# Kernel tuning notes

Measured on AMD Instinct MI355X. Metric: run time of the kernel, lower is better.

## Reference

```python
import jax, jax.numpy as jnp
import numpy as np

B, T, C, H = 2, 2048, 1024, 16
HD = C // H
HID = C * 4 // 3  # 1365, SwiGLU hidden
EPS = 1e-5


def _ln(x, g, b):
    m = x.mean(-1, keepdims=True)
    v = ((x - m) ** 2).mean(-1, keepdims=True)
    return (x - m) / jnp.sqrt(v + EPS) * g + b


def setup_inputs() -> dict:
    key0 = jax.random.key(0)
    ks = jax.random.split(key0, 16)
    s = 0.02
    inp = {
        'query': jax.random.normal(ks[0], (B, T, C), jnp.float32),
        'key': jax.random.normal(ks[1], (B, T, C), jnp.float32),
        'g_q': jnp.ones((C,), jnp.float32), 'b_q': jnp.zeros((C,), jnp.float32),
        'g_k': jnp.ones((C,), jnp.float32), 'b_k': jnp.zeros((C,), jnp.float32),
        'in_proj_w': jax.random.normal(ks[2], (3 * C, C), jnp.float32) * s,
        'in_proj_b': jnp.zeros((3 * C,), jnp.float32),
        'out_w': jax.random.normal(ks[3], (C, C), jnp.float32) * s,
        'out_b': jnp.zeros((C,), jnp.float32),
        'proj_w': jax.random.normal(ks[4], (C, C), jnp.float32) * s,
        'proj_b': jnp.zeros((C,), jnp.float32),
        'rel_table': jax.random.normal(ks[5], (H, 2 * 2048 - 1), jnp.float32) * s,
        'g_ffn': jnp.ones((C,), jnp.float32), 'b_ffn': jnp.zeros((C,), jnp.float32),
        'w1': jax.random.normal(ks[6], (HID, C), jnp.float32) * s,
        'w2': jax.random.normal(ks[7], (HID, C), jnp.float32) * s,
        'w3': jax.random.normal(ks[8], (C, HID), jnp.float32) * s,
        'g_out': jnp.ones((C,), jnp.float32), 'b_out': jnp.zeros((C,), jnp.float32),
        'max_len': 2048,
    }
    return inp


def reference(query, key, g_q, b_q, g_k, b_k, in_proj_w, in_proj_b, out_w, out_b,
              proj_w, proj_b, rel_table, g_ffn, b_ffn, w1, w2, w3, g_out, b_out, max_len):
    Tq, Tk = query.shape[1], key.shape[1]
    q = _ln(query, g_q, b_q)
    k = _ln(key, g_k, b_k)
    # in-projection (torch MHA packed weights)
    wq, wk, wv = jnp.split(in_proj_w, 3, axis=0)
    bq, bk, bv = jnp.split(in_proj_b, 3, axis=0)
    qp = (q @ wq.T + bq).reshape(B, Tq, H, HD).transpose(0, 2, 1, 3)
    kp = (k @ wk.T + bk).reshape(B, Tk, H, HD).transpose(0, 2, 1, 3)
    vp = (k @ wv.T + bv).reshape(B, Tk, H, HD).transpose(0, 2, 1, 3)
    # relative-position bias, mean over heads -> [Tq,Tk] additive mask
    rel_idx = jnp.clip(jnp.arange(Tq)[:, None] - jnp.arange(Tk)[None, :] + (max_len - 1),
                       0, 2 * max_len - 2)
    mask = rel_table[:, rel_idx].mean(axis=0)  # [Tq,Tk]
    scores = jnp.einsum('bhqd,bhkd->bhqk', qp, kp) / jnp.sqrt(jnp.float32(HD))
    attn = jax.nn.softmax(scores + mask[None, None], axis=-1)
    ctx = jnp.einsum('bhqk,bhkd->bhqd', attn, vp)
    ctx = ctx.transpose(0, 2, 1, 3).reshape(B, Tq, C)
    attn_out = ctx @ out_w.T + out_b
    attn_out = attn_out @ proj_w.T + proj_b
    x = query + attn_out
    # SwiGLU FFN (proj dropout/dropout are identity at eval)
    h = _ln(x, g_ffn, b_ffn)
    ff = (jax.nn.silu(h @ w1.T) * (h @ w2.T)) @ w3.T
    x = x + ff
    return _ln(x, g_out, b_out)
```

## Files before the change

kernel.cpp:

```cpp
#include <hip/hip_runtime.h>
#include <hip/hip_bf16.h>

static constexpr int Bb  = 2;
static constexpr int Tt  = 2048;
static constexpr int Cc  = 1024;
static constexpr int Hh  = 16;
static constexpr int HDi = 64;
static constexpr int HID = 1365;
static constexpr int HIDP = 1408;
static constexpr int Mm  = Bb * Tt;

typedef unsigned short u16;
typedef __attribute__((ext_vector_type(8))) short bf16x8;
typedef __attribute__((ext_vector_type(4))) float f32x4;
typedef __attribute__((ext_vector_type(8))) unsigned short u16x8;
typedef __attribute__((ext_vector_type(4))) unsigned short u16x4;

__device__ inline u16 f2bf(float f) {
    unsigned u = __builtin_bit_cast(unsigned, f);
    u += 0x7fffu + ((u >> 16) & 1u);
    return (u16)(u >> 16);
}

__device__ inline unsigned cvtpk(float lo, float hi) {
    unsigned r;
    asm("v_cvt_pk_bf16_f32 %0, %1, %2" : "=v"(r) : "v"(lo), "v"(hi));
    return r;
}

__device__ inline float vexp2(float x) {
    float r;
    asm("v_exp_f32 %0, %1" : "=v"(r) : "v"(x));
    return r;
}

__device__ inline void gl16(const void* g, void* l) {
    __builtin_amdgcn_global_load_lds(
        (const __attribute__((address_space(1))) unsigned*)g,
        (__attribute__((address_space(3))) unsigned*)l, 16, 0, 0);
}

template<int OUTBF>
__global__ __launch_bounds__(256) void ln_k(const float* __restrict__ x,
                                            const float* __restrict__ g,
                                            const float* __restrict__ b,
                                            void* __restrict__ yv) {
    int row = blockIdx.x;
    int tid = threadIdx.x;
    const float4* xr = (const float4*)(x + (size_t)row * Cc);
    float4 v = xr[tid];
    float s  = v.x + v.y + v.z + v.w;
    float ss = v.x*v.x + v.y*v.y + v.z*v.z + v.w*v.w;
    __shared__ float rs[256], rq[256];
    rs[tid] = s; rq[tid] = ss;
    __syncthreads();
    for (int o = 128; o > 0; o >>= 1) {
        if (tid < o) { rs[tid] += rs[tid+o]; rq[tid] += rq[tid+o]; }
        __syncthreads();
    }
    float mean = rs[0] * (1.f/Cc);
    float var  = rq[0] * (1.f/Cc) - mean*mean;
    float inv  = rsqrtf(var + 1e-5f);
    float4 gv = ((const float4*)g)[tid];
    float4 bv = ((const float4*)b)[tid];
    float o0 = (v.x-mean)*inv*gv.x + bv.x;
    float o1 = (v.y-mean)*inv*gv.y + bv.y;
    float o2 = (v.z-mean)*inv*gv.z + bv.z;
    float o3 = (v.w-mean)*inv*gv.w + bv.w;
    if (OUTBF) {
        u16x4 o4 = { f2bf(o0), f2bf(o1), f2bf(o2), f2bf(o3) };
        ((u16x4*)((u16*)yv + (size_t)row * Cc))[tid] = o4;
    } else {
        float4 o4 = { o0, o1, o2, o3 };
        ((float4*)((float*)yv + (size_t)row * Cc))[tid] = o4;
    }
}

__global__ __launch_bounds__(256) void ln2_k(const float* __restrict__ q,
                                             const float* __restrict__ k,
                                             const float* __restrict__ gq, const float* __restrict__ bq,
                                             const float* __restrict__ gk, const float* __restrict__ bk,
                                             u16* __restrict__ qn, u16* __restrict__ kn) {
    int row = blockIdx.x;
    const float* x; const float* g; const float* bb; u16* y; int r;
    if (row < Mm) { x = q; g = gq; bb = bq; y = qn; r = row; }
    else          { x = k; g = gk; bb = bk; y = kn; r = row - Mm; }
    int tid = threadIdx.x;
    float4 v = ((const float4*)(x + (size_t)r * Cc))[tid];
    float s  = v.x + v.y + v.z + v.w;
    float ss = v.x*v.x + v.y*v.y + v.z*v.z + v.w*v.w;
    __shared__ float rs[256], rq2[256];
    rs[tid] = s; rq2[tid] = ss;
    __syncthreads();
    for (int o = 128; o > 0; o >>= 1) {
        if (tid < o) { rs[tid] += rs[tid+o]; rq2[tid] += rq2[tid+o]; }
        __syncthreads();
    }
    float mean = rs[0] * (1.f/Cc);
    float var  = rq2[0] * (1.f/Cc) - mean*mean;
    float inv  = rsqrtf(var + 1e-5f);
    float4 gv = ((const float4*)g)[tid];
    float4 bv = ((const float4*)bb)[tid];
    u16x4 o4 = { f2bf((v.x-mean)*inv*gv.x + bv.x), f2bf((v.y-mean)*inv*gv.y + bv.y),
                 f2bf((v.z-mean)*inv*gv.z + bv.z), f2bf((v.w-mean)*inv*gv.w + bv.w) };
    ((u16x4*)(y + (size_t)r * Cc))[tid] = o4;
}

__global__ __launch_bounds__(256) void prep_k(const float* __restrict__ in_proj_w, u16* __restrict__ wA,
                                              const float* __restrict__ proj_w,  u16* __restrict__ wPb,
                                              const float* __restrict__ w1, u16* __restrict__ w1b,
                                              const float* __restrict__ w2, u16* __restrict__ w2b,
                                              const float* __restrict__ w3, u16* __restrict__ w3b,
                                              const float* __restrict__ out_w, u16* __restrict__ wOt,
                                              const float* __restrict__ out_b, const float* __restrict__ bp,
                                              float* __restrict__ bc,
                                              const float* __restrict__ rel, float* __restrict__ mr) {
    __shared__ float sh[64*65];
    int bid = blockIdx.x, tid = threadIdx.x;
    if (bid < 3456) {
        int u = bid * 256 + tid;
        const float* src; u16* dst; int valid;
        if (u < 1536*256)                   { src = in_proj_w; dst = wA;  valid = 3*Cc*Cc; }
        else if ((u -= 1536*256) < 512*256) { src = proj_w;    dst = wPb; valid = Cc*Cc; }
        else if ((u -= 512*256) < 704*256)  { src = w1;        dst = w1b; valid = HID*Cc; }
        else     { u -= 704*256;              src = w2;        dst = w2b; valid = HID*Cc; }
        int e0 = u * 8;
        u16x8 o;
        if (e0 + 8 <= valid) {
            float4 a = *(const float4*)(src + e0);
            float4 b = *(const float4*)(src + e0 + 4);
            o[0]=f2bf(a.x); o[1]=f2bf(a.y); o[2]=f2bf(a.z); o[3]=f2bf(a.w);
            o[4]=f2bf(b.x); o[5]=f2bf(b.y); o[6]=f2bf(b.z); o[7]=f2bf(b.w);
        } else {
            #pragma unroll
            for (int j = 0; j < 8; j++) { int e = e0 + j; o[j] = f2bf(e < valid ? src[e] : 0.f); }
        }
        *(u16x8*)(dst + (size_t)e0) = o;
    } else if (bid < 4160) {
        int idx = (bid - 3456) * 256 + tid;
        int e0 = idx * 8;
        int r = e0 / HIDP, c0 = e0 - r * HIDP;
        u16x8 o;
        #pragma unroll
        for (int j = 0; j < 8; j++) {
            int c = c0 + j;
            o[j] = f2bf(c < HID ? w3[(size_t)r * HID + c] : 0.f);
        }
        *(u16x8*)(w3b + (size_t)e0) = o;
    } else if (bid < 4416) {
        int id = bid - 4160;
        int j0 = (id & 15) * 64, c0 = (id >> 4) * 64;
        #pragma unroll
        for (int i = 0; i < 16; i++) {
            int e = tid + i*256;
            int c = e >> 6, j = e & 63;
            sh[c*65 + j] = out_w[(size_t)(c0 + c) * Cc + j0 + j];
        }
        __syncthreads();
        #pragma unroll
        for (int i = 0; i < 16; i++) {
            int e = tid + i*256;
            int j = e >> 6, c = e & 63;
            wOt[(size_t)(j0 + j) * Cc + c0 + c] = f2bf(sh[c*65 + j]);
        }
    } else if (bid < 5440) {
        int i = bid - 4416;
        float4 w = ((const float4*)(proj_w + (size_t)i * Cc))[tid];
        float4 b = ((const float4*)out_b)[tid];
        float s = w.x*b.x + w.y*b.y + w.z*b.z + w.w*b.w;
        sh[tid] = s; __syncthreads();
        for (int o = 128; o > 0; o >>= 1) {
            if (tid < o) sh[tid] += sh[tid+o];
            __syncthreads();
        }
        if (tid == 0) bc[i] = sh[0] + bp[i];
    } else {
        int j = (bid - 5440) * 256 + tid;
        if (j < 2*Tt - 1) {
            float s = 0.f;
            #pragma unroll
            for (int h = 0; h < Hh; h++) s += rel[(size_t)h * (2*Tt - 1) + j];
            mr[j] = s * (1.f/Hh);
        }
    }
}

template<int OUTBF, int HASRES, int HASBIAS>
__global__ __launch_bounds__(256) void mgemm64_k(const u16* __restrict__ A,
                                                 const u16* __restrict__ W,
                                                 const float* __restrict__ bias,
                                                 const float* __restrict__ res,
                                                 void* __restrict__ outv,
                                                 int N, int K) {
    __shared__ u16 As[2][64*32];
    __shared__ u16 Ws[2][128*32];
    int bm = blockIdx.y * 64, bn = blockIdx.x * 128;
    int tid = threadIdx.x, w = tid >> 6, l = tid & 63;
    int lr = l & 15, lh = l >> 4;
    int wm = (w >> 1) * 32, wn = (w & 1) * 64;
    f32x4 acc[2][4] = {};

    auto stage = [&](int buf, int kt) {
        {
            int row = tid >> 2, slot = tid & 3;
            int ko = kt + ((slot ^ (row & 3)) << 3);
            gl16(A + (size_t)(bm + row) * K + ko, (char*)As[buf] + tid * 16);
        }
        #pragma unroll
        for (int c = 0; c < 2; c++) {
            int i = c*256 + tid;
            int row = i >> 2, slot = i & 3;
            int ko = kt + ((slot ^ (row & 3)) << 3);
            gl16(W + (size_t)(bn + row) * K + ko, (char*)Ws[buf] + (c*256 + tid) * 16);
        }
    };
    stage(0, 0);
    for (int kt = 0; kt < K; kt += 32) {
        int buf = (kt >> 5) & 1;
        __syncthreads();
        if (kt + 32 < K) stage(buf ^ 1, kt + 32);
        bf16x8 af[2], wf[4];
        #pragma unroll
        for (int f = 0; f < 2; f++) {
            int r = wm + f*16 + lr;
            af[f] = *(const bf16x8*)((const char*)As[buf] + r*64 + ((lh ^ (r & 3)) << 4));
        }
        #pragma unroll
        for (int f = 0; f < 4; f++) {
            int rn = wn + f*16 + lr;
            wf[f] = *(const bf16x8*)((const char*)Ws[buf] + rn*64 + ((lh ^ (rn & 3)) << 4));
        }
        #pragma unroll
        for (int fm = 0; fm < 2; fm++)
            #pragma unroll
            for (int fn = 0; fn < 4; fn++)
                acc[fm][fn] = __builtin_amdgcn_mfma_f32_16x16x32_bf16(af[fm], wf[fn], acc[fm][fn], 0, 0, 0);
    }

    #pragma unroll
    for (int fm = 0; fm < 2; fm++) {
        #pragma unroll
        for (int r = 0; r < 4; r++) {
            int row = bm + wm + fm*16 + lh*4 + r;
            #pragma unroll
            for (int fn = 0; fn < 4; fn++) {
                int col = bn + wn + fn*16 + lr;
                float v = acc[fm][fn][r];
                if (HASBIAS) v += bias[col];
                if (HASRES)  v += res[(size_t)row * N + col];
                if (OUTBF) ((u16*)outv)[(size_t)row * N + col] = f2bf(v);
                else       ((float*)outv)[(size_t)row * N + col] = v;
            }
        }
    }
}

__global__ __launch_bounds__(256) void mqkv_k(const u16* __restrict__ qn,
                                              const u16* __restrict__ kn,
                                              const u16* __restrict__ wA,
                                              const float* __restrict__ bias3,
                                              u16* __restrict__ out3,
                                              const u16* __restrict__ wPb,
                                              const u16* __restrict__ wOt,
                                              u16* __restrict__ wCb) {
    int z = blockIdx.z;
    const u16* A; const u16* W; const float* bias = bias3; u16* out;
    if (z < 3) { A = z ? kn : qn; W = wA + (size_t)z * Cc * Cc; bias = bias3 + z * Cc; out = out3 + (size_t)z * Mm * Cc; }
    else       { if (blockIdx.y >= 8) return; A = wPb; W = wOt; out = wCb; }

    __shared__ u16 As[2][128*32];
    __shared__ u16 Ws[2][128*32];
    int bm = blockIdx.y * 128, bn = blockIdx.x * 128;
    int tid = threadIdx.x, w = tid >> 6, l = tid & 63;
    int lr = l & 15, lh = l >> 4;
    int wm = (w >> 1) * 64, wn = (w & 1) * 64;
    f32x4 acc[4][4] = {};

    auto stage = [&](int buf, int kt) {
        #pragma unroll
        for (int c = 0; c < 2; c++) {
            int i = w*128 + c*64 + l;
            int row = i >> 2, slot = i & 3;
            int ko = kt + ((slot ^ (row & 3)) << 3);
            gl16(A + (size_t)(bm + row) * Cc + ko, (char*)As[buf] + (w*128 + c*64) * 16);
            gl16(W + (size_t)(bn + row) * Cc + ko, (char*)Ws[buf] + (w*128 + c*64) * 16);
        }
    };
    stage(0, 0);
    for (int kt = 0; kt < Cc; kt += 32) {
        int buf = (kt >> 5) & 1;
        __syncthreads();
        if (kt + 32 < Cc) stage(buf ^ 1, kt + 32);
        bf16x8 af[4], wf[4];
        #pragma unroll
        for (int f = 0; f < 4; f++) {
            int r = wm + f*16 + lr;
            af[f] = *(const bf16x8*)((const char*)As[buf] + r*64 + ((lh ^ (r & 3)) << 4));
            int rn = wn + f*16 + lr;
            wf[f] = *(const bf16x8*)((const char*)Ws[buf] + rn*64 + ((lh ^ (rn & 3)) << 4));
        }
        #pragma unroll
        for (int fm = 0; fm < 4; fm++)
            #pragma unroll
            for (int fn = 0; fn < 4; fn++)
                acc[fm][fn] = __builtin_amdgcn_mfma_f32_16x16x32_bf16(af[fm], wf[fn], acc[fm][fn], 0, 0, 0);
    }

    #pragma unroll
    for (int fm = 0; fm < 4; fm++) {
        #pragma unroll
        for (int r = 0; r < 4; r++) {
            int row = bm + wm + fm*16 + lh*4 + r;
            #pragma unroll
            for (int fn = 0; fn < 4; fn++) {
                int col = bn + wn + fn*16 + lr;
                float v = acc[fm][fn][r];
                if (z < 3) v += bias[col];
                out[(size_t)row * Cc + col] = f2bf(v);
            }
        }
    }
}

__global__ __launch_bounds__(256) void mswiglu64_k(const u16* __restrict__ A,
                                                   const u16* __restrict__ W1,
                                                   const u16* __restrict__ W2,
                                                   u16* __restrict__ out,
                                                   int N, int K) {
    __shared__ u16 As[2][64*32];
    __shared__ u16 W1s[2][128*32];
    __shared__ u16 W2s[2][128*32];
    int bm = blockIdx.y * 64, bn = blockIdx.x * 128;
    int tid = threadIdx.x, w = tid >> 6, l = tid & 63;
    int lr = l & 15, lh = l >> 4;
    int wm = (w >> 1) * 32, wn = (w & 1) * 64;
    f32x4 acc1[2][4] = {};
    f32x4 acc2[2][4] = {};

    auto stage = [&](int buf, int kt) {
        {
            int row = tid >> 2, slot = tid & 3;
            int ko = kt + ((slot ^ (row & 3)) << 3);
            gl16(A + (size_t)(bm + row) * K + ko, (char*)As[buf] + tid * 16);
        }
        #pragma unroll
        for (int c = 0; c < 2; c++) {
            int i = c*256 + tid;
            int row = i >> 2, slot = i & 3;
            int ko = kt + ((slot ^ (row & 3)) << 3);
            gl16(W1 + (size_t)(bn + row) * K + ko, (char*)W1s[buf] + (c*256 + tid) * 16);
            gl16(W2 + (size_t)(bn + row) * K + ko, (char*)W2s[buf] + (c*256 + tid) * 16);
        }
    };
    stage(0, 0);
    for (int kt = 0; kt < K; kt += 32) {
        int buf = (kt >> 5) & 1;
        __syncthreads();
        if (kt + 32 < K) stage(buf ^ 1, kt + 32);
        bf16x8 af[2], w1f[4], w2f[4];
        #pragma unroll
        for (int f = 0; f < 2; f++) {
            int r = wm + f*16 + lr;
            af[f] = *(const bf16x8*)((const char*)As[buf] + r*64 + ((lh ^ (r & 3)) << 4));
        }
        #pragma unroll
        for (int f = 0; f < 4; f++) {
            int rn = wn + f*16 + lr;
            int offn = rn*64 + ((lh ^ (rn & 3)) << 4);
            w1f[f] = *(const bf16x8*)((const char*)W1s[buf] + offn);
            w2f[f] = *(const bf16x8*)((const char*)W2s[buf] + offn);
        }
        #pragma unroll
        for (int fm = 0; fm < 2; fm++)
            #pragma unroll
            for (int fn = 0; fn < 4; fn++) {
                acc1[fm][fn] = __builtin_amdgcn_mfma_f32_16x16x32_bf16(af[fm], w1f[fn], acc1[fm][fn], 0, 0, 0);
                acc2[fm][fn] = __builtin_amdgcn_mfma_f32_16x16x32_bf16(af[fm], w2f[fn], acc2[fm][fn], 0, 0, 0);
            }
    }

    #pragma unroll
    for (int fm = 0; fm < 2; fm++) {
        #pragma unroll
        for (int r = 0; r < 4; r++) {
            int row = bm + wm + fm*16 + lh*4 + r;
            #pragma unroll
            for (int fn = 0; fn < 4; fn++) {
                int col = bn + wn + fn*16 + lr;
                float a = acc1[fm][fn][r];
                float sig = 1.f / (1.f + __expf(-a));
                out[(size_t)row * N + col] = f2bf(a * sig * acc2[fm][fn][r]);
            }
        }
    }
}

__global__ __launch_bounds__(256) void vt_k(const u16* __restrict__ vp,
                                            u16* __restrict__ vt) {
    int blk = blockIdx.x;
    int bh = blk >> 5, kb = blk & 31;
    int b = bh >> 4, h = bh & 15;
    __shared__ u16 t[64][65];
    int tid = threadIdx.x;
    size_t bc = (size_t)b*Tt*Cc + (size_t)h*HDi;
    #pragma unroll
    for (int i = 0; i < 16; i++) {
        int e = tid + i*256;
        int k = e >> 6, d = e & 63;
        t[d][k] = vp[bc + (size_t)(kb*64 + k)*Cc + d];
    }
    __syncthreads();
    #pragma unroll
    for (int i = 0; i < 16; i++) {
        int e = tid + i*256;
        int d = e >> 6, k = e & 63;
        vt[((size_t)bh*64 + d)*Tt + kb*64 + k] = t[d][k];
    }
}

__global__ __launch_bounds__(512) void fattn_k(const u16* __restrict__ qp,
                                               const u16* __restrict__ kp,
                                               const u16* __restrict__ vt,
                                               const float* __restrict__ mr,
                                               u16* __restrict__ ctx) {
    __shared__ alignas(128) u16 Kt[2*4096];
    __shared__ alignas(128) u16 Vts[2*4096];
    __shared__ float mrw[2176];

    constexpr float C1 = 0.18033688011118324f;

    int bid = blockIdx.x;
    int blk = ((bid & 7) << 6) | (bid >> 3);
    int qt = blk & 15, h = (blk >> 4) & 15, b = blk >> 8;
    int q0 = qt * 128;
    int tid = threadIdx.x, w = tid >> 6, l = tid & 63;
    int lr = l & 15, lh = l >> 4;
    size_t bc = (size_t)b * Tt * Cc + (size_t)h * HDi;
    const u16* vtb = vt + (size_t)(b*Hh + h) * HDi * Tt;

    for (int i = tid; i < 2175; i += 512) mrw[i] = mr[q0 + i] * 8.f;

    bf16x8 qa[2];
    {
        const u16* qrow = qp + bc + (size_t)(q0 + w*16 + lr) * Cc;
        qa[0] = *(const bf16x8*)(qrow + lh*8);
        qa[1] = *(const bf16x8*)(qrow + 32 + lh*8);
    }

    f32x4 oacc[4] = {};
    float mrun = -1e30f, lrun = 0.f;

    const char* pKb0 = (const char*)Kt + (lr>>2)*1024 + (lr&3)*128
                       + ((lh ^ (lr & 3)) << 4) + (((lr >> 2) & 1) << 6);
    const char* pKb1 = (const char*)((size_t)pKb0 ^ 64);
    int g6 = ((((lr >> 2) ^ (lr >> 3)) & 1) << 6);
    const char* pV0 = (const char*)Vts + lr*128 + ((lh ^ (lr & 3)) << 4) + g6;
    const char* pV1 = (const char*)((size_t)pV0 ^ 64);
    const char* pm = (const char*)mrw + (w*16 + lr - lh*8 + 2047 - 39) * 4;

    int sl = tid & 7, kr0 = tid >> 3;
    int so = (sl ^ (kr0 & 7) ^ (((kr0 >> 3) & 1) << 2)) << 3;
    const u16* gK = kp + bc + (size_t)kr0 * Cc + so;
    const u16* gV = vtb + (size_t)kr0 * Tt + so;
    int wb = (tid & 448) * 16;
    char* dK0 = (char*)Kt  + wb;
    char* dV0 = (char*)Vts + wb;

    auto stage = [&](int bufo) {
        gl16(gK, dK0 + bufo);
        gl16(gV, dV0 + bufo);
        gK += 64*Cc;
        gV += 64;
    };

    auto tile = [&](int bufo) {
        f32x4 s[4];
        #pragma unroll
        for (int f = 0; f < 4; f++) {
            int ob = 39 - (f & 1)*32 - (f >> 1)*4;
            s[f][0] = *(const float*)(pm + (ob    ) * 4);
            s[f][1] = *(const float*)(pm + (ob - 1) * 4);
            s[f][2] = *(const float*)(pm + (ob - 2) * 4);
            s[f][3] = *(const float*)(pm + (ob - 3) * 4);
        }
        pm -= 256;
        __builtin_amdgcn_s_setprio(1);
        {
            const char* k0 = pKb0 + bufo;
            const char* k1 = pKb1 + bufo;
            bf16x8 kb;
            kb = *(const bf16x8*)(k0 + 0);    s[0] = __builtin_amdgcn_mfma_f32_16x16x32_bf16(kb, qa[0], s[0], 0, 0, 0);
            kb = *(const bf16x8*)(k1 + 0);    s[0] = __builtin_amdgcn_mfma_f32_16x16x32_bf16(kb, qa[1], s[0], 0, 0, 0);
            kb = *(const bf16x8*)(k0 + 4096); s[1] = __builtin_amdgcn_mfma_f32_16x16x32_bf16(kb, qa[0], s[1], 0, 0, 0);
            kb = *(const bf16x8*)(k1 + 4096); s[1] = __builtin_amdgcn_mfma_f32_16x16x32_bf16(kb, qa[1], s[1], 0, 0, 0);
            kb = *(const bf16x8*)(k1 + 512);  s[2] = __builtin_amdgcn_mfma_f32_16x16x32_bf16(kb, qa[0], s[2], 0, 0, 0);
            kb = *(const bf16x8*)(k0 + 512);  s[2] = __builtin_amdgcn_mfma_f32_16x16x32_bf16(kb, qa[1], s[2], 0, 0, 0);
            kb = *(const bf16x8*)(k1 + 4608); s[3] = __builtin_amdgcn_mfma_f32_16x16x32_bf16(kb, qa[0], s[3], 0, 0, 0);
            kb = *(const bf16x8*)(k0 + 4608); s[3] = __builtin_amdgcn_mfma_f32_16x16x32_bf16(kb, qa[1], s[3], 0, 0, 0);
        }
        __builtin_amdgcn_s_setprio(0);

        float tm = -1e30f;
        #pragma unroll
        for (int f = 0; f < 4; f++)
            #pragma unroll
            for (int r = 0; r < 4; r++) tm = fmaxf(tm, s[f][r]);
        tm = fmaxf(tm, __shfl_xor(tm, 16));
        tm = fmaxf(tm, __shfl_xor(tm, 32));

        float corr = 1.f;
        bool nod = __all(tm <= mrun + 64.f);
        if (!nod) {
            float mn = fmaxf(mrun, tm);
            corr = vexp2((mrun - mn) * C1);
            mrun = mn;
        }
        float mnc = mrun * C1;
        float ts = 0.f;
        #pragma unroll
        for (int f = 0; f < 4; f++)
            #pragma unroll
            for (int r = 0; r < 4; r++) {
                float e = vexp2(fmaf(s[f][r], C1, -mnc));
                s[f][r] = e; ts += e;
            }
        ts += __shfl_xor(ts, 16);
        ts += __shfl_xor(ts, 32);
        if (nod) {
            lrun += ts;
        } else {
            lrun = lrun*corr + ts;
            #pragma unroll
            for (int f = 0; f < 4; f++) {
                oacc[f][0] *= corr; oacc[f][1] *= corr;
                oacc[f][2] *= corr; oacc[f][3] *= corr;
            }
        }

        uint4 pb0u = { cvtpk(s[0][0], s[0][1]), cvtpk(s[0][2], s[0][3]),
                       cvtpk(s[2][0], s[2][1]), cvtpk(s[2][2], s[2][3]) };
        uint4 pb1u = { cvtpk(s[1][0], s[1][1]), cvtpk(s[1][2], s[1][3]),
                       cvtpk(s[3][0], s[3][1]), cvtpk(s[3][2], s[3][3]) };
        bf16x8 pb0 = __builtin_bit_cast(bf16x8, pb0u);
        bf16x8 pb1 = __builtin_bit_cast(bf16x8, pb1u);

        __builtin_amdgcn_s_setprio(1);
        #pragma unroll
        for (int f = 0; f < 4; f++) {
            bf16x8 vb0 = *(const bf16x8*)(pV0 + bufo + f*2048);
            oacc[f] = __builtin_amdgcn_mfma_f32_16x16x32_bf16(vb0, pb0, oacc[f], 0, 0, 0);
            bf16x8 vb1 = *(const bf16x8*)(pV1 + bufo + f*2048);
            oacc[f] = __builtin_amdgcn_mfma_f32_16x16x32_bf16(vb1, pb1, oacc[f], 0, 0, 0);
        }
        __builtin_amdgcn_s_setprio(0);
    };

    stage(0);
    #pragma unroll 1
    for (int kt = 0; kt < 32; kt += 2) {
        __syncthreads();
        stage(8192);
        tile(0);
        __syncthreads();
        if (kt < 30) stage(0);
        tile(8192);
    }

    float iv = 1.f / lrun;
    size_t rowoff = bc + (size_t)(q0 + w*16 + lr) * Cc;
    #pragma unroll
    for (int f = 0; f < 4; f++) {
        u16x4 o4 = { f2bf(oacc[f][0]*iv), f2bf(oacc[f][1]*iv),
                     f2bf(oacc[f][2]*iv), f2bf(oacc[f][3]*iv) };
        *(u16x4*)(ctx + rowoff + f*16 + lh*4) = o4;
    }
}

extern "C" void kernel_launch(void* const* d_in, const int* in_sizes, int n_in,
                              void* d_out, int out_size, void* d_ws, size_t ws_size,
                              hipStream_t stream) {
    const float* query     = (const float*)d_in[0];
    const float* key       = (const float*)d_in[1];
    const float* g_q       = (const float*)d_in[2];
    const float* b_q       = (const float*)d_in[3];
    const float* g_k       = (const float*)d_in[4];
    const float* b_k       = (const float*)d_in[5];
    const float* in_proj_w = (const float*)d_in[6];
    const float* in_proj_b = (const float*)d_in[7];
    const float* out_w     = (const float*)d_in[8];
    const float* out_b     = (const float*)d_in[9];
    const float* proj_w    = (const float*)d_in[10];
    const float* proj_b    = (const float*)d_in[11];
    const float* rel_table = (const float*)d_in[12];
    const float* g_ffn     = (const float*)d_in[13];
    const float* b_ffn     = (const float*)d_in[14];
    const float* w1        = (const float*)d_in[15];
    const float* w2        = (const float*)d_in[16];
    const float* w3        = (const float*)d_in[17];
    const float* g_out     = (const float*)d_in[18];
    const float* b_out     = (const float*)d_in[19];

    char* p = (char*)d_ws;
    auto alloc = [&](size_t bytes) { char* r = p; p += bytes; return r; };
    const size_t MCb = (size_t)Mm * Cc * 2;
    u16* wA  = (u16*)alloc((size_t)3*Cc*Cc*2);
    u16* wPb = (u16*)alloc((size_t)Cc*Cc*2);
    u16* wOt = (u16*)alloc((size_t)Cc*Cc*2);
    u16* wCb = (u16*)alloc((size_t)Cc*Cc*2);
    u16* w1b = (u16*)alloc((size_t)HIDP*Cc*2);
    u16* w2b = (u16*)alloc((size_t)HIDP*Cc*2);
    u16* w3b = (u16*)alloc((size_t)Cc*HIDP*2);
    float* bc = (float*)alloc(Cc*4);
    float* mr = (float*)alloc(4096*4);
    u16* qn = (u16*)alloc(MCb);
    u16* kn = (u16*)alloc(MCb);
    u16* qp = (u16*)alloc(MCb);
    u16* kp = (u16*)alloc(MCb);
    u16* vp = (u16*)alloc(MCb);
    u16* vt = (u16*)alloc(MCb);
    float* x  = (float*)alloc((size_t)Mm*Cc*4);
    float* x2 = (float*)alloc((size_t)Mm*Cc*4);
    u16* ctx = qn;
    u16* h   = qp;
    u16* gf  = vp;

    dim3 blk(256);
    prep_k<<<5456, blk, 0, stream>>>(in_proj_w, wA, proj_w, wPb, w1, w1b, w2, w2b,
                                     w3, w3b, out_w, wOt, out_b, proj_b, bc, rel_table, mr);

    ln2_k<<<2*Mm, blk, 0, stream>>>(query, key, g_q, b_q, g_k, b_k, qn, kn);

    dim3 gqkv(Cc/128, Mm/128, 4);
    mqkv_k<<<gqkv, blk, 0, stream>>>(qn, kn, wA, in_proj_b, qp, wPb, wOt, wCb);

    vt_k<<<Bb*Hh*32, blk, 0, stream>>>(vp, vt);
    fattn_k<<<Bb*Hh*16, dim3(512), 0, stream>>>(qp, kp, vt, mr, ctx);

    dim3 g1(Cc/128, Mm/64);
    mgemm64_k<0,1,1><<<g1, blk, 0, stream>>>(ctx, wCb, bc, query, x, Cc, Cc);

    ln_k<1><<<Mm, blk, 0, stream>>>(x, g_ffn, b_ffn, h);
    dim3 g2(HIDP/128, Mm/64);
    mswiglu64_k<<<g2, blk, 0, stream>>>(h, w1b, w2b, gf, HIDP, Cc);
    dim3 g3(Cc/128, Mm/64);
    mgemm64_k<0,1,0><<<g3, blk, 0, stream>>>(gf, w3b, nullptr, x, x2, Cc, HIDP);

    ln_k<0><<<Mm, blk, 0, stream>>>(x2, g_out, b_out, d_out);
}
```

Baseline: 256.9 us.

## Fuse LN into prep kernel, remap QKV grid for XCDs, widen attention KV tile

The query/key layernorm kernel is merged into the weight-prep kernel, which saves one launch. The QKV GEMM now uses a 1D grid of 832 blocks whose block IDs are remapped so neighbouring tiles land on the same XCD, and it drops the dead blocks the old z=3 slice produced. The flash-attention kernel processes 128 keys per iteration instead of 64, doubling the K/V LDS buffers and halving the number of loop iterations and barriers. The larger LDS footprint and register count may lower occupancy.

```diff
diff --git a/kernel.cpp b/kernel.cpp
--- a/kernel.cpp
+++ b/kernel.cpp
@@ -76,47 +76,47 @@
     }
 }
 
-__global__ __launch_bounds__(256) void ln2_k(const float* __restrict__ q,
-                                             const float* __restrict__ k,
-                                             const float* __restrict__ gq, const float* __restrict__ bq,
-                                             const float* __restrict__ gk, const float* __restrict__ bk,
-                                             u16* __restrict__ qn, u16* __restrict__ kn) {
-    int row = blockIdx.x;
-    const float* x; const float* g; const float* bb; u16* y; int r;
-    if (row < Mm) { x = q; g = gq; bb = bq; y = qn; r = row; }
-    else          { x = k; g = gk; bb = bk; y = kn; r = row - Mm; }
-    int tid = threadIdx.x;
-    float4 v = ((const float4*)(x + (size_t)r * Cc))[tid];
-    float s  = v.x + v.y + v.z + v.w;
-    float ss = v.x*v.x + v.y*v.y + v.z*v.z + v.w*v.w;
-    __shared__ float rs[256], rq2[256];
-    rs[tid] = s; rq2[tid] = ss;
-    __syncthreads();
-    for (int o = 128; o > 0; o >>= 1) {
-        if (tid < o) { rs[tid] += rs[tid+o]; rq2[tid] += rq2[tid+o]; }
-        __syncthreads();
-    }
-    float mean = rs[0] * (1.f/Cc);
-    float var  = rq2[0] * (1.f/Cc) - mean*mean;
-    float inv  = rsqrtf(var + 1e-5f);
-    float4 gv = ((const float4*)g)[tid];
-    float4 bv = ((const float4*)bb)[tid];
-    u16x4 o4 = { f2bf((v.x-mean)*inv*gv.x + bv.x), f2bf((v.y-mean)*inv*gv.y + bv.y),
-                 f2bf((v.z-mean)*inv*gv.z + bv.z), f2bf((v.w-mean)*inv*gv.w + bv.w) };
-    ((u16x4*)(y + (size_t)r * Cc))[tid] = o4;
-}
-
-__global__ __launch_bounds__(256) void prep_k(const float* __restrict__ in_proj_w, u16* __restrict__ wA,
-                                              const float* __restrict__ proj_w,  u16* __restrict__ wPb,
-                                              const float* __restrict__ w1, u16* __restrict__ w1b,
-                                              const float* __restrict__ w2, u16* __restrict__ w2b,
-                                              const float* __restrict__ w3, u16* __restrict__ w3b,
-                                              const float* __restrict__ out_w, u16* __restrict__ wOt,
-                                              const float* __restrict__ out_b, const float* __restrict__ bp,
-                                              float* __restrict__ bc,
-                                              const float* __restrict__ rel, float* __restrict__ mr) {
+__global__ __launch_bounds__(256) void prepln_k(const float* __restrict__ query,
+                                                const float* __restrict__ key,
+                                                const float* __restrict__ gq, const float* __restrict__ bq,
+                                                const float* __restrict__ gk, const float* __restrict__ bk,
+                                                u16* __restrict__ qn, u16* __restrict__ kn,
+                                                const float* __restrict__ in_proj_w, u16* __restrict__ wA,
+                                                const float* __restrict__ proj_w,  u16* __restrict__ wPb,
+                                                const float* __restrict__ w1, u16* __restrict__ w1b,
+                                                const float* __restrict__ w2, u16* __restrict__ w2b,
+                                                const float* __restrict__ w3, u16* __restrict__ w3b,
+                                                const float* __restrict__ out_w, u16* __restrict__ wOt,
+                                                const float* __restrict__ out_b, const float* __restrict__ bp,
+                                                float* __restrict__ bc,
+                                                const float* __restrict__ rel, float* __restrict__ mr) {
     __shared__ float sh[64*65];
     int bid = blockIdx.x, tid = threadIdx.x;
+    if (bid < 2*Mm) {
+        const float* x; const float* g; const float* bb; u16* y; int r;
+        if (bid < Mm) { x = query; g = gq; bb = bq; y = qn; r = bid; }
+        else          { x = key;   g = gk; bb = bk; y = kn; r = bid - Mm; }
+        float4 v = ((const float4*)(x + (size_t)r * Cc))[tid];
+        float s  = v.x + v.y + v.z + v.w;
+        float ss = v.x*v.x + v.y*v.y + v.z*v.z + v.w*v.w;
+        float* rs = sh; float* rq2 = sh + 256;
+        rs[tid] = s; rq2[tid] = ss;
+        __syncthreads();
+        for (int o = 128; o > 0; o >>= 1) {
+            if (tid < o) { rs[tid] += rs[tid+o]; rq2[tid] += rq2[tid+o]; }
+            __syncthreads();
+        }
+        float mean = rs[0] * (1.f/Cc);
+        float var  = rq2[0] * (1.f/Cc) - mean*mean;
+        float inv  = rsqrtf(var + 1e-5f);
+        float4 gv = ((const float4*)g)[tid];
+        float4 bv = ((const float4*)bb)[tid];
+        u16x4 o4 = { f2bf((v.x-mean)*inv*gv.x + bv.x), f2bf((v.y-mean)*inv*gv.y + bv.y),
+                     f2bf((v.z-mean)*inv*gv.z + bv.z), f2bf((v.w-mean)*inv*gv.w + bv.w) };
+        ((u16x4*)(y + (size_t)r * Cc))[tid] = o4;
+        return;
+    }
+    bid -= 2*Mm;
     if (bid < 3456) {
         int u = bid * 256 + tid;
         const float* src; u16* dst; int valid;
@@ -263,14 +263,24 @@
                                               const u16* __restrict__ wPb,
                                               const u16* __restrict__ wOt,
                                               u16* __restrict__ wCb) {
-    int z = blockIdx.z;
-    const u16* A; const u16* W; const float* bias = bias3; u16* out;
-    if (z < 3) { A = z ? kn : qn; W = wA + (size_t)z * Cc * Cc; bias = bias3 + z * Cc; out = out3 + (size_t)z * Mm * Cc; }
-    else       { if (blockIdx.y >= 8) return; A = wPb; W = wOt; out = wCb; }
-
     __shared__ u16 As[2][128*32];
     __shared__ u16 Ws[2][128*32];
-    int bm = blockIdx.y * 128, bn = blockIdx.x * 128;
+
+    int bid = blockIdx.x;
+    int xcd = bid & 7, j = bid >> 3;
+    int p = xcd * 13 + (j >> 3), x = j & 7;
+    const u16* A; const u16* W; const float* bias = bias3; u16* out;
+    int bm, bn = x * 128, hasb;
+    if (p < 96) {
+        int z = p >> 5, y = p & 31;
+        A = z ? kn : qn; W = wA + (size_t)z * Cc * Cc;
+        bias = bias3 + z * Cc; out = out3 + (size_t)z * Mm * Cc;
+        bm = y * 128; hasb = 1;
+    } else {
+        A = wPb; W = wOt; out = wCb;
+        bm = (p - 96) * 128; hasb = 0;
+    }
+
     int tid = threadIdx.x, w = tid >> 6, l = tid & 63;
     int lr = l & 15, lh = l >> 4;
     int wm = (w >> 1) * 64, wn = (w & 1) * 64;
@@ -310,13 +320,13 @@
     for (int fm = 0; fm < 4; fm++) {
         #pragma unroll
         for (int r = 0; r < 4; r++) {
-            int row = bm + wm + fm*16 + lh*4 + r;
+            int orow = bm + wm + fm*16 + lh*4 + r;
             #pragma unroll
             for (int fn = 0; fn < 4; fn++) {
                 int col = bn + wn + fn*16 + lr;
                 float v = acc[fm][fn][r];
-                if (z < 3) v += bias[col];
-                out[(size_t)row * Cc + col] = f2bf(v);
+                if (hasb) v += bias[col];
+                out[(size_t)orow * Cc + col] = f2bf(v);
             }
         }
     }
@@ -423,8 +433,8 @@
                                                const u16* __restrict__ vt,
                                                const float* __restrict__ mr,
                                                u16* __restrict__ ctx) {
-    __shared__ alignas(128) u16 Kt[2*4096];
-    __shared__ alignas(128) u16 Vts[2*4096];
+    __shared__ alignas(128) u16 Kt[2*8192];
+    __shared__ alignas(128) u16 Vts[2*8192];
     __shared__ float mrw[2176];
 
     constexpr float C1 = 0.18033688011118324f;
@@ -453,56 +463,71 @@
     const char* pKb0 = (const char*)Kt + (lr>>2)*1024 + (lr&3)*128
                        + ((lh ^ (lr & 3)) << 4) + (((lr >> 2) & 1) << 6);
     const char* pKb1 = (const char*)((size_t)pKb0 ^ 64);
-    int g6 = ((((lr >> 2) ^ (lr >> 3)) & 1) << 6);
-    const char* pV0 = (const char*)Vts + lr*128 + ((lh ^ (lr & 3)) << 4) + g6;
-    const char* pV1 = (const char*)((size_t)pV0 ^ 64);
-    const char* pm = (const char*)mrw + (w*16 + lr - lh*8 + 2047 - 39) * 4;
-
-    int sl = tid & 7, kr0 = tid >> 3;
-    int so = (sl ^ (kr0 & 7) ^ (((kr0 >> 3) & 1) << 2)) << 3;
-    const u16* gK = kp + bc + (size_t)kr0 * Cc + so;
-    const u16* gV = vtb + (size_t)kr0 * Tt + so;
+    int cr2 = lr >> 2;
+    const char* pVb = (const char*)Vts + lr*256 + ((lh ^ (lr & 3)) << 4);
+    const char* pVc0 = pVb + (((0 ^ cr2) & 3) << 6);
+    const char* pVc1 = pVb + (((1 ^ cr2) & 3) << 6);
+    const char* pVc2 = pVb + (((2 ^ cr2) & 3) << 6);
+    const char* pVc3 = pVb + (((3 ^ cr2) & 3) << 6);
+    const char* pm = (const char*)mrw + (w*16 + lr - lh*8 + 2047 - 103) * 4;
+
+    int ksl = tid & 7, kr0 = tid >> 3;
+    int so_k = (ksl ^ (kr0 & 7) ^ (((kr0 >> 3) & 1) << 2)) << 3;
+    const u16* gK = kp + bc + (size_t)kr0 * Cc + so_k;
+    int vsl = tid & 15, vr0 = tid >> 4;
+    int so_v = (vsl ^ (vr0 & 15)) << 3;
+    const u16* gV = vtb + (size_t)vr0 * Tt + so_v;
     int wb = (tid & 448) * 16;
     char* dK0 = (char*)Kt  + wb;
     char* dV0 = (char*)Vts + wb;
 
     auto stage = [&](int bufo) {
-        gl16(gK, dK0 + bufo);
-        gl16(gV, dV0 + bufo);
-        gK += 64*Cc;
-        gV += 64;
+        gl16(gK,                      dK0 + bufo);
+        gl16(gK + (size_t)64*Cc,      dK0 + bufo + 8192);
+        gl16(gV,                      dV0 + bufo);
+        gl16(gV + (size_t)32*Tt,      dV0 + bufo + 8192);
+        gK += 128*Cc;
+        gV += 128;
     };
 
     auto tile = [&](int bufo) {
-        f32x4 s[4];
-        #pragma unroll
-        for (int f = 0; f < 4; f++) {
-            int ob = 39 - (f & 1)*32 - (f >> 1)*4;
+        f32x4 s[8];
+        #pragma unroll
+        for (int f = 0; f < 8; f++) {
+            int ob = 103 - (f & 1)*32 - ((f >> 1) & 1)*4 - (f >> 2)*64;
             s[f][0] = *(const float*)(pm + (ob    ) * 4);
             s[f][1] = *(const float*)(pm + (ob - 1) * 4);
             s[f][2] = *(const float*)(pm + (ob - 2) * 4);
             s[f][3] = *(const float*)(pm + (ob - 3) * 4);
         }
-        pm -= 256;
+        pm -= 512;
         __builtin_amdgcn_s_setprio(1);
         {
             const char* k0 = pKb0 + bufo;
             const char* k1 = pKb1 + bufo;
             bf16x8 kb;
-            kb = *(const bf16x8*)(k0 + 0);    s[0] = __builtin_amdgcn_mfma_f32_16x16x32_bf16(kb, qa[0], s[0], 0, 0, 0);
-            kb = *(const bf16x8*)(k1 + 0);    s[0] = __builtin_amdgcn_mfma_f32_16x16x32_bf16(kb, qa[1], s[0], 0, 0, 0);
-            kb = *(const bf16x8*)(k0 + 4096); s[1] = __builtin_amdgcn_mfma_f32_16x16x32_bf16(kb, qa[0], s[1], 0, 0, 0);
-            kb = *(const bf16x8*)(k1 + 4096); s[1] = __builtin_amdgcn_mfma_f32_16x16x32_bf16(kb, qa[1], s[1], 0, 0, 0);
-            kb = *(const bf16x8*)(k1 + 512);  s[2] = __builtin_amdgcn_mfma_f32_16x16x32_bf16(kb, qa[0], s[2], 0, 0, 0);
-            kb = *(const bf16x8*)(k0 + 512);  s[2] = __builtin_amdgcn_mfma_f32_16x16x32_bf16(kb, qa[1], s[2], 0, 0, 0);
-            kb = *(const bf16x8*)(k1 + 4608); s[3] = __builtin_amdgcn_mfma_f32_16x16x32_bf16(kb, qa[0], s[3], 0, 0, 0);
-            kb = *(const bf16x8*)(k0 + 4608); s[3] = __builtin_amdgcn_mfma_f32_16x16x32_bf16(kb, qa[1], s[3], 0, 0, 0);
+            kb = *(const bf16x8*)(k0 + 0);     s[0] = __builtin_amdgcn_mfma_f32_16x16x32_bf16(kb, qa[0], s[0], 0, 0, 0);
+            kb = *(const bf16x8*)(k1 + 0);     s[0] = __builtin_amdgcn_mfma_f32_16x16x32_bf16(kb, qa[1], s[0], 0, 0, 0);
+            kb = *(const bf16x8*)(k0 + 4096);  s[1] = __builtin_amdgcn_mfma_f32_16x16x32_bf16(kb, qa[0], s[1], 0, 0, 0);
+            kb = *(const bf16x8*)(k1 + 4096);  s[1] = __builtin_amdgcn_mfma_f32_16x16x32_bf16(kb, qa[1], s[1], 0, 0, 0);
+            kb = *(const bf16x8*)(k1 + 512);   s[2] = __builtin_amdgcn_mfma_f32_16x16x32_bf16(kb, qa[0], s[2], 0, 0, 0);
+            kb = *(const bf16x8*)(k0 + 512);   s[2] = __builtin_amdgcn_mfma_f32_16x16x32_bf16(kb, qa[1], s[2], 0, 0, 0);
+            kb = *(const bf16x8*)(k1 + 4608);  s[3] = __builtin_amdgcn_mfma_f32_16x16x32_bf16(kb, qa[0], s[3], 0, 0, 0);
+            kb = *(const bf16x8*)(k0 + 4608);  s[3] = __builtin_amdgcn_mfma_f32_16x16x32_bf16(kb, qa[1], s[3], 0, 0, 0);
+            kb = *(const bf16x8*)(k0 + 8192);  s[4] = __builtin_amdgcn_mfma_f32_16x16x32_bf16(kb, qa[0], s[4], 0, 0, 0);
+            kb = *(const bf16x8*)(k1 + 8192);  s[4] = __builtin_amdgcn_mfma_f32_16x16x32_bf16(kb, qa[1], s[4], 0, 0, 0);
+            kb = *(const bf16x8*)(k0 + 12288); s[5] = __builtin_amdgcn_mfma_f32_16x16x32_bf16(kb, qa[0], s[5], 0, 0, 0);
+            kb = *(const bf16x8*)(k1 + 12288); s[5] = __builtin_amdgcn_mfma_f32_16x16x32_bf16(kb, qa[1], s[5], 0, 0, 0);
+            kb = *(const bf16x8*)(k1 + 8704);  s[6] = __builtin_amdgcn_mfma_f32_16x16x32_bf16(kb, qa[0], s[6], 0, 0, 0);
+            kb = *(const bf16x8*)(k0 + 8704);  s[6] = __builtin_amdgcn_mfma_f32_16x16x32_bf16(kb, qa[1], s[6], 0, 0, 0);
+            kb = *(const bf16x8*)(k1 + 12800); s[7] = __builtin_amdgcn_mfma_f32_16x16x32_bf16(kb, qa[0], s[7], 0, 0, 0);
+            kb = *(const bf16x8*)(k0 + 12800); s[7] = __builtin_amdgcn_mfma_f32_16x16x32_bf16(kb, qa[1], s[7], 0, 0, 0);
         }
         __builtin_amdgcn_s_setprio(0);
 
         float tm = -1e30f;
         #pragma unroll
-        for (int f = 0; f < 4; f++)
+        for (int f = 0; f < 8; f++)
             #pragma unroll
             for (int r = 0; r < 4; r++) tm = fmaxf(tm, s[f][r]);
         tm = fmaxf(tm, __shfl_xor(tm, 16));
@@ -518,7 +543,7 @@
         float mnc = mrun * C1;
         float ts = 0.f;
         #pragma unroll
-        for (int f = 0; f < 4; f++)
+        for (int f = 0; f < 8; f++)
             #pragma unroll
             for (int r = 0; r < 4; r++) {
                 float e = vexp2(fmaf(s[f][r], C1, -mnc));
@@ -541,29 +566,40 @@
                        cvtpk(s[2][0], s[2][1]), cvtpk(s[2][2], s[2][3]) };
         uint4 pb1u = { cvtpk(s[1][0], s[1][1]), cvtpk(s[1][2], s[1][3]),
                        cvtpk(s[3][0], s[3][1]), cvtpk(s[3][2], s[3][3]) };
+        uint4 pb2u = { cvtpk(s[4][0], s[4][1]), cvtpk(s[4][2], s[4][3]),
+                       cvtpk(s[6][0], s[6][1]), cvtpk(s[6][2], s[6][3]) };
+        uint4 pb3u = { cvtpk(s[5][0], s[5][1]), cvtpk(s[5][2], s[5][3]),
+                       cvtpk(s[7][0], s[7][1]), cvtpk(s[7][2], s[7][3]) };
         bf16x8 pb0 = __builtin_bit_cast(bf16x8, pb0u);
         bf16x8 pb1 = __builtin_bit_cast(bf16x8, pb1u);
+        bf16x8 pb2 = __builtin_bit_cast(bf16x8, pb2u);
+        bf16x8 pb3 = __builtin_bit_cast(bf16x8, pb3u);
 
         __builtin_amdgcn_s_setprio(1);
         #pragma unroll
-        for (int f = 0; f < 4; f++) {
-            bf16x8 vb0 = *(const bf16x8*)(pV0 + bufo + f*2048);
-            oacc[f] = __builtin_amdgcn_mfma_f32_16x16x32_bf16(vb0, pb0, oacc[f], 0, 0, 0);
-            bf16x8 vb1 = *(const bf16x8*)(pV1 + bufo + f*2048);
-            oacc[f] = __builtin_amdgcn_mfma_f32_16x16x32_bf16(vb1, pb1, oacc[f], 0, 0, 0);
+        for (int ff = 0; ff < 4; ff++) {
+            bf16x8 vb;
+            vb = *(const bf16x8*)(pVc0 + bufo + ff*4096);
+            oacc[ff] = __builtin_amdgcn_mfma_f32_16x16x32_bf16(vb, pb0, oacc[ff], 0, 0, 0);
+            vb = *(const bf16x8*)(pVc1 + bufo + ff*4096);
+            oacc[ff] = __builtin_amdgcn_mfma_f32_16x16x32_bf16(vb, pb1, oacc[ff], 0, 0, 0);
+            vb = *(const bf16x8*)(pVc2 + bufo + ff*4096);
+            oacc[ff] = __builtin_amdgcn_mfma_f32_16x16x32_bf16(vb, pb2, oacc[ff], 0, 0, 0);
+            vb = *(const bf16x8*)(pVc3 + bufo + ff*4096);
+            oacc[ff] = __builtin_amdgcn_mfma_f32_16x16x32_bf16(vb, pb3, oacc[ff], 0, 0, 0);
         }
         __builtin_amdgcn_s_setprio(0);
     };
 
     stage(0);
     #pragma unroll 1
-    for (int kt = 0; kt < 32; kt += 2) {
-        __syncthreads();
-        stage(8192);
+    for (int kt = 0; kt < 16; kt += 2) {
+        __syncthreads();
+        stage(16384);
         tile(0);
         __syncthreads();
-        if (kt < 30) stage(0);
-        tile(8192);
+        if (kt < 14) stage(0);
+        tile(16384);
     }
 
     float iv = 1.f / lrun;
@@ -625,13 +661,11 @@
     u16* gf  = vp;
 
     dim3 blk(256);
-    prep_k<<<5456, blk, 0, stream>>>(in_proj_w, wA, proj_w, wPb, w1, w1b, w2, w2b,
-                                     w3, w3b, out_w, wOt, out_b, proj_b, bc, rel_table, mr);
-
-    ln2_k<<<2*Mm, blk, 0, stream>>>(query, key, g_q, b_q, g_k, b_k, qn, kn);
-
-    dim3 gqkv(Cc/128, Mm/128, 4);
-    mqkv_k<<<gqkv, blk, 0, stream>>>(qn, kn, wA, in_proj_b, qp, wPb, wOt, wCb);
+    prepln_k<<<2*Mm + 5456, blk, 0, stream>>>(query, key, g_q, b_q, g_k, b_k, qn, kn,
+                                              in_proj_w, wA, proj_w, wPb, w1, w1b, w2, w2b,
+                                              w3, w3b, out_w, wOt, out_b, proj_b, bc, rel_table, mr);
+
+    mqkv_k<<<832, blk, 0, stream>>>(qn, kn, wA, in_proj_b, qp, wPb, wOt, wCb);
 
     vt_k<<<Bb*Hh*32, blk, 0, stream>>>(vp, vt);
     fattn_k<<<Bb*Hh*16, dim3(512), 0, stream>>>(qp, kp, vt, mr, ctx);
```

After: 252.4 us. Within noise of the previous version (-1.8%).
